# Performance work log

Measured on AMD Instinct MI355X. Metric: run time of the kernel, lower is better.

The kernel has to match this reference:

```python
import jax, jax.numpy as jnp
import numpy as np

N = 50000
IN_CH = 128
OUT_CH = 64
H1, C1 = 8, 8


def gat_layer(x, src, dst, W, att_src, att_dst, bias, heads, out_ch, concat, n_nodes):
    # x: [N, F_in]; W: [F_in, heads*out_ch]; att_*: [heads, out_ch]; bias: [heads*out_ch] or [out_ch]
    h = (x @ W).reshape(n_nodes, heads, out_ch)              # [N,H,C]
    a_src = jnp.einsum('nhc,hc->nh', h, att_src)             # [N,H]
    a_dst = jnp.einsum('nhc,hc->nh', h, att_dst)             # [N,H]
    e = jax.nn.leaky_relu(a_src[src] + a_dst[dst], 0.2)      # [E,H]
    # segment softmax over incoming edges of each dst node
    m = jax.ops.segment_max(e, dst, num_segments=n_nodes)    # [N,H]
    p = jnp.exp(e - m[dst])                                  # [E,H]
    s = jax.ops.segment_sum(p, dst, num_segments=n_nodes)    # [N,H]
    alpha = p / (s[dst] + 1e-16)                             # [E,H]
    out = jax.ops.segment_sum(h[src] * alpha[:, :, None], dst, num_segments=n_nodes)  # [N,H,C]
    out = out.reshape(n_nodes, heads * out_ch) if concat else out.mean(axis=1)
    return out + bias


def setup_inputs() -> dict:
    key = jax.random.key(0)
    ks = jax.random.split(key, 12)
    E = 1600000
    x = jax.random.normal(ks[0], (N, IN_CH), dtype=jnp.float32)
    edge_index = jax.random.randint(ks[1], (2, E), 0, N, dtype=jnp.int64)
    sc = 0.1
    return {
        'x': x,
        'edge_index': edge_index,
        'W1': jax.random.normal(ks[2], (IN_CH, H1 * C1), dtype=jnp.float32) * sc,
        'att_src1': jax.random.normal(ks[3], (H1, C1), dtype=jnp.float32) * sc,
        'att_dst1': jax.random.normal(ks[4], (H1, C1), dtype=jnp.float32) * sc,
        'b1': jnp.zeros((H1 * C1,), dtype=jnp.float32),
        'W2': jax.random.normal(ks[5], (H1 * C1, OUT_CH), dtype=jnp.float32) * sc,
        'att_src2': jax.random.normal(ks[6], (1, OUT_CH), dtype=jnp.float32) * sc,
        'att_dst2': jax.random.normal(ks[7], (1, OUT_CH), dtype=jnp.float32) * sc,
        'b2': jnp.zeros((OUT_CH,), dtype=jnp.float32),
        'lin_W': jax.random.normal(ks[8], (OUT_CH, 1), dtype=jnp.float32) * sc,
        'lin_b': jnp.zeros((1,), dtype=jnp.float32),
    }


def reference(x, edge_index, W1, att_src1, att_dst1, b1, W2, att_src2, att_dst2, b2, lin_W, lin_b):
    # add self loops (PyG GATConv default)
    loops = jnp.arange(N, dtype=edge_index.dtype)
    src = jnp.concatenate([edge_index[0], loops])
    dst = jnp.concatenate([edge_index[1], loops])
    # dropout layers are identity in eval mode
    h = gat_layer(x, src, dst, W1, att_src1, att_dst1, b1, H1, C1, True, N)
    h = jax.nn.elu(h)
    h = gat_layer(h, src, dst, W2, att_src2, att_dst2, b2, 1, OUT_CH, False, N)
    return h @ lin_W + lin_b
```

## Files before the change

### kernel.cpp

```cpp
#include <hip/hip_runtime.h>
#include <hip/hip_bf16.h>
#include <math.h>

#define NN     50000
#define FIN    128
#define F1     64
#define NH1    8
#define F2     64

#define BSH    256
#define NB     ((NN + BSH - 1) / BSH)
#define BCAP   9472
#define PREB   13
#define MG1B   ((NN + 255) / 256)

typedef __bf16 bf16x8 __attribute__((ext_vector_type(8)));
typedef float  f32x4  __attribute__((ext_vector_type(4)));


__device__ __forceinline__ float loadF(const void* p, long long i, int fp32) {
    if (fp32) return ((const float*)p)[i];
    return __bfloat162float(((const __hip_bfloat16*)p)[i]);
}
__device__ __forceinline__ int loadI_nt(const void* p, long long i, int i64) {
    if (i64) return (int)__builtin_nontemporal_load(&((const long long*)p)[i]);
    return __builtin_nontemporal_load(&((const int*)p)[i]);
}
__device__ __forceinline__ unsigned short f2bfu(float f) {
    unsigned u = __float_as_uint(f);
    return (unsigned short)((u + 0x7FFFu + ((u >> 16) & 1u)) >> 16);
}
__device__ __forceinline__ float b2f(unsigned short u) {
    return __uint_as_float(((unsigned)u) << 16);
}


__global__ __launch_bounds__(1024) void k_front(
    const void* __restrict__ x, const void* __restrict__ ei, int E, int Etot,
    int* __restrict__ flags,
    const void* __restrict__ W1, const void* __restrict__ W2,
    unsigned short* __restrict__ W1p, unsigned short* __restrict__ W2p,
    int* __restrict__ bcnt, unsigned* __restrict__ binned) {
    __shared__ int s_a, s_b;
    __shared__ int hist[NB], gbase[NB];
    int tid = threadIdx.x;
    if (blockIdx.x < PREB) {
        if (tid == 0) { s_a = 0; s_b = 0; }
        __syncthreads();
        const unsigned short* u = (const unsigned short*)x;
        int cnt = 0;
        for (int i = tid; i < 8192; i += 1024) {
            unsigned short v = u[i];
            if ((v & 0x7F80) == 0x7F80) cnt++;
        }
        if (cnt) atomicAdd(&s_a, cnt);
        const unsigned* e32 = (const unsigned*)ei;
        int nz = 0;
        for (int i = tid; i < 2048; i += 1024) {
            if (e32[2 * i + 1] != 0u) nz++;
        }
        if (nz) atomicAdd(&s_b, nz);
        __syncthreads();
        int fp32 = (s_a > 2) ? 1 : 0;
        if (tid == 0 && blockIdx.x == 0) {
            flags[0] = fp32;
            flags[1] = (s_b == 0) ? 1 : 0;
        }
        int gt = blockIdx.x * 1024 + tid, gs = PREB * 1024;
        for (int i = gt; i < (FIN / 32) * 4 * 512; i += gs) {
            int j = i & 7, l = (i >> 3) & 63, f = i >> 9;
            int kb = f >> 2, nt = f & 3;
            int k = kb * 32 + (l >> 4) * 8 + j, n = nt * 16 + (l & 15);
            W1p[i] = f2bfu(loadF(W1, k * 64 + n, fp32));
        }
        for (int i = gt; i < (F1 / 32) * 4 * 512; i += gs) {
            int j = i & 7, l = (i >> 3) & 63, f = i >> 9;
            int kb = f >> 2, nt = f & 3;
            int k = kb * 32 + (l >> 4) * 8 + j, n = nt * 16 + (l & 15);
            W2p[i] = f2bfu(loadF(W2, k * 64 + n, fp32));
        }
    } else {
        if (tid == 0) s_b = 0;
        for (int i = tid; i < NB; i += 1024) hist[i] = 0;
        __syncthreads();
        const unsigned* e32 = (const unsigned*)ei;
        int nz = 0;
        for (int i = tid; i < 2048; i += 1024) {
            if (e32[2 * i + 1] != 0u) nz++;
        }
        if (nz) atomicAdd(&s_b, nz);
        __syncthreads();
        int i64 = (s_b == 0) ? 1 : 0;
        long long base = (long long)(blockIdx.x - PREB) * 8192;
        unsigned pk[8]; short bb[8];
        #pragma unroll
        for (int u = 0; u < 8; ++u) {
            long long j = base + u * 1024 + tid;
            int s = -1, d = -1;
            if (j < Etot) {
                if (j < E) { s = loadI_nt(ei, j, i64); d = loadI_nt(ei, (long long)E + j, i64); }
                else       { s = d = (int)(j - E); }
            }
            if ((unsigned)s < NN && (unsigned)d < NN) {
                bb[u] = (short)(d >> 8);
                pk[u] = ((unsigned)s << 8) | (unsigned)(d & 255);
                atomicAdd(&hist[bb[u]], 1);
            } else bb[u] = -1;
        }
        __syncthreads();
        for (int i = tid; i < NB; i += 1024) {
            int h = hist[i];
            gbase[i] = h ? atomicAdd(&bcnt[i], h) : 0;
            hist[i] = 0;
        }
        __syncthreads();
        #pragma unroll
        for (int u = 0; u < 8; ++u) {
            if (bb[u] >= 0) {
                int pos = gbase[bb[u]] + atomicAdd(&hist[bb[u]], 1);
                if (pos < BCAP) binned[(size_t)bb[u] * BCAP + pos] = pk[u];
            }
        }
    }
}


__global__ __launch_bounds__(1024) void k_mid(
    const int* __restrict__ bcnt, const unsigned* __restrict__ binned,
    int* __restrict__ offs, int* __restrict__ perm,
    const void* __restrict__ x, const unsigned short* __restrict__ W1p,
    const void* __restrict__ attS, const void* __restrict__ attD,
    __hip_bfloat16* __restrict__ h1, float* __restrict__ a1s,
    float* __restrict__ a1d, const int* __restrict__ flags) {
    __shared__ __align__(16) char smem[33280];
    int tid = threadIdx.x;
    if (blockIdx.x < NB) {
        int* hist = (int*)smem;
        int* cur  = (int*)(smem + 1024);
        int* sd   = (int*)(smem + 2048);
        int bk = blockIdx.x;
        int n0 = bk * BSH;
        if (tid < 256) sd[tid] = (tid < NB) ? min(bcnt[tid], BCAP) : 0;
        __syncthreads();
        for (int off = 1; off < BSH; off <<= 1) {
            int t = 0;
            if (tid < 256 && tid >= off) t = sd[tid - off];
            __syncthreads();
            if (tid < 256) sd[tid] += t;
            __syncthreads();
        }
        int gb = (bk > 0) ? sd[bk - 1] : 0;
        if (bk == 0 && tid == 0) offs[NN] = sd[NB - 1];
        __syncthreads();
        int cnt = bcnt[bk]; if (cnt > BCAP) cnt = BCAP;
        const unsigned* bp = binned + (size_t)bk * BCAP;
        if (tid < 256) hist[tid] = 0;
        __syncthreads();
        for (int i = tid; i < cnt; i += 1024)
            atomicAdd(&hist[bp[i] & 255], 1);
        __syncthreads();
        int myh = (tid < 256) ? hist[tid] : 0;
        if (tid < 256) sd[tid] = myh;
        __syncthreads();
        for (int off = 1; off < BSH; off <<= 1) {
            int t = 0;
            if (tid < 256 && tid >= off) t = sd[tid - off];
            __syncthreads();
            if (tid < 256) sd[tid] += t;
            __syncthreads();
        }
        if (tid < 256) {
            int excl = sd[tid] - myh;
            cur[tid] = gb + excl;
            if (n0 + tid < NN) offs[n0 + tid] = gb + excl;
        }
        __syncthreads();
        for (int i = tid; i < cnt; i += 1024) {
            unsigned pk = bp[i];
            int pos = atomicAdd(&cur[pk & 255], 1);
            perm[pos] = (int)(pk >> 8);
        }
    } else {
        int fp32 = flags[0];
        unsigned short* hl = (unsigned short*)smem;
        float* attSl = (float*)(smem + 32768);
        float* attDl = (float*)(smem + 32768 + 256);
        if (tid < 64) { attSl[tid] = loadF(attS, tid, fp32); attDl[tid] = loadF(attD, tid, fp32); }
        int sub = tid >> 8, t = tid & 255;
        int w = t >> 6, l = t & 63;
        int quad = l >> 4, lm = l & 15;
        int n0 = (blockIdx.x - NB) * 256 + sub * 64;
        unsigned short* hls = hl + sub * 4096;

        bf16x8 bfr[16];
        #pragma unroll
        for (int f = 0; f < 16; ++f)
            bfr[f] = *(const bf16x8*)(W1p + f * 512 + l * 8);

        int nodeA = n0 + w * 16 + lm;
        long long rowA = (nodeA < NN) ? nodeA : 0;
        f32x4 acc[4];
        #pragma unroll
        for (int nt = 0; nt < 4; ++nt) acc[nt] = (f32x4){0.f, 0.f, 0.f, 0.f};

        #pragma unroll
        for (int kb = 0; kb < 4; ++kb) {
            bf16x8 af;
            if (!fp32) {
                af = *(const bf16x8*)((const unsigned short*)x + rowA * FIN + kb * 32 + quad * 8);
            } else {
                const float* xf = (const float*)x + rowA * FIN + kb * 32 + quad * 8;
                union { unsigned short s[8]; bf16x8 v; } tmp;
                #pragma unroll
                for (int j = 0; j < 8; ++j) tmp.s[j] = f2bfu(xf[j]);
                af = tmp.v;
            }
            #pragma unroll
            for (int nt = 0; nt < 4; ++nt)
                acc[nt] = __builtin_amdgcn_mfma_f32_16x16x32_bf16(af, bfr[kb * 4 + nt], acc[nt], 0, 0, 0);
        }

        #pragma unroll
        for (int nt = 0; nt < 4; ++nt) {
            #pragma unroll
            for (int r = 0; r < 4; ++r) {
                int nl = w * 16 + quad * 4 + r;
                int node = n0 + nl;
                int c = nt * 16 + lm;
                unsigned short hb = f2bfu(acc[nt][r]);
                hls[nl * 64 + c] = hb;
                if (node < NN) ((unsigned short*)h1)[(size_t)node * 64 + c] = hb;
            }
        }
        __syncthreads();
        #pragma unroll
        for (int pp = 0; pp < 2; ++pp) {
            int p = t + pp * 256;
            int nl = p >> 3, g = p & 7;
            int node = n0 + nl;
            float ss = 0.f, dd = 0.f;
            #pragma unroll
            for (int j = 0; j < 8; ++j) {
                float hv = b2f(hls[nl * 64 + g * 8 + j]);
                ss += hv * attSl[g * 8 + j];
                dd += hv * attDl[g * 8 + j];
            }
            if (node < NN) {
                a1s[(size_t)node * NH1 + g] = ss;
                a1d[(size_t)node * NH1 + g] = dd;
            }
        }
    }
}


#define HLP 72

__global__ __launch_bounds__(256) void k_agg1f(
    const int* __restrict__ offs, const int* __restrict__ perm,
    const __hip_bfloat16* __restrict__ h1, const float* __restrict__ a1s,
    const float* __restrict__ a1d, const void* __restrict__ b1,
    const unsigned short* __restrict__ W2p,
    const void* __restrict__ attS2, const void* __restrict__ attD2,
    const void* __restrict__ linW,
    float2* __restrict__ g2s, float* __restrict__ a2d,
    int n, const int* __restrict__ flags) {
    int fp32 = flags[0];
    __shared__ unsigned short hl[16 * HLP];
    __shared__ float attSl[64], attDl[64];
    __shared__ float sp[16 * 4], dp[16 * 4], gp[16 * 4];
    int tid = threadIdx.x;
    if (tid < 64) { attSl[tid] = loadF(attS2, tid, fp32); attDl[tid] = loadF(attD2, tid, fp32); }
    int w = tid >> 6, c = tid & 63;
    int n0 = blockIdx.x * 16;
    int u = c & 7, h = c >> 3, cb = c & 56;
    const unsigned short* hu = (const unsigned short*)h1;

    for (int m = 0; m < 4; ++m) {
        int d = n0 + w * 4 + m;
        if (d < n) {
            int start = offs[d], end = offs[d + 1];
            float adl = a1d[(size_t)d * NH1 + h];
            float acc = 0.f, denp = 0.f;
            for (int i = start; i < end; i += 8) {
                int j = i + u;
                int jc = (j < end) ? j : (end - 1);
                int sj = perm[jc];
                float e = a1s[(size_t)sj * NH1 + h] + adl;
                e = fmaxf(e, 0.2f * e);
                float p = (j < end) ? __expf(e) : 0.f;
                denp += p;
                #pragma unroll
                for (int k = 0; k < 8; ++k) {
                    int su = __builtin_amdgcn_readlane(sj, k);
                    float pk = __shfl(p, cb + k, 64);
                    acc = fmaf(pk, b2f(hu[(size_t)su * 64 + c]), acc);
                }
            }
            denp += __shfl_xor(denp, 1, 64);
            denp += __shfl_xor(denp, 2, 64);
            denp += __shfl_xor(denp, 4, 64);
            float v = acc / (denp + 1e-16f) + loadF(b1, c, fp32);
            v = (v > 0.f) ? v : expm1f(v);
            hl[(w * 4 + m) * HLP + c] = f2bfu(v);
        }
    }
    __syncthreads();

    int quad = c >> 4, lm = c & 15;
    bf16x8 bf0 = *(const bf16x8*)(W2p + (0 * 4 + w) * 512 + c * 8);
    bf16x8 bf1 = *(const bf16x8*)(W2p + (1 * 4 + w) * 512 + c * 8);
    bf16x8 af0 = *(const bf16x8*)(hl + lm * HLP + 0 * 32 + quad * 8);
    bf16x8 af1 = *(const bf16x8*)(hl + lm * HLP + 1 * 32 + quad * 8);
    f32x4 acc2 = (f32x4){0.f, 0.f, 0.f, 0.f};
    acc2 = __builtin_amdgcn_mfma_f32_16x16x32_bf16(af0, bf0, acc2, 0, 0, 0);
    acc2 = __builtin_amdgcn_mfma_f32_16x16x32_bf16(af1, bf1, acc2, 0, 0, 0);

    int cg = w * 16 + lm;
    float aSc = attSl[cg], aDc = attDl[cg];
    float lWc = loadF(linW, cg, fp32);
    #pragma unroll
    for (int r = 0; r < 4; ++r) {
        int nl = quad * 4 + r;
        unsigned short hb = f2bfu(acc2[r]);
        float hv = b2f(hb);
        float pvs = hv * aSc, pvd = hv * aDc, pvg = hv * lWc;
        pvs += __shfl_xor(pvs, 1, 64); pvd += __shfl_xor(pvd, 1, 64); pvg += __shfl_xor(pvg, 1, 64);
        pvs += __shfl_xor(pvs, 2, 64); pvd += __shfl_xor(pvd, 2, 64); pvg += __shfl_xor(pvg, 2, 64);
        pvs += __shfl_xor(pvs, 4, 64); pvd += __shfl_xor(pvd, 4, 64); pvg += __shfl_xor(pvg, 4, 64);
        pvs += __shfl_xor(pvs, 8, 64); pvd += __shfl_xor(pvd, 8, 64); pvg += __shfl_xor(pvg, 8, 64);
        if (lm == 0) { sp[nl * 4 + w] = pvs; dp[nl * 4 + w] = pvd; gp[nl * 4 + w] = pvg; }
    }
    __syncthreads();
    if (tid < 16) {
        int node = n0 + tid;
        if (node < n) {
            float ss = sp[tid * 4 + 0] + sp[tid * 4 + 1] + sp[tid * 4 + 2] + sp[tid * 4 + 3];
            float dd = dp[tid * 4 + 0] + dp[tid * 4 + 1] + dp[tid * 4 + 2] + dp[tid * 4 + 3];
            float gg = gp[tid * 4 + 0] + gp[tid * 4 + 1] + gp[tid * 4 + 2] + gp[tid * 4 + 3];
            g2s[node] = make_float2(ss, gg);
            a2d[node] = dd;
        }
    }
}


__global__ __launch_bounds__(256) void k_agg2(
    const int* __restrict__ offs, const int* __restrict__ perm,
    const float2* __restrict__ g2s, const float* __restrict__ a2d,
    const void* __restrict__ b2, const void* __restrict__ linW,
    const void* __restrict__ linb,
    void* __restrict__ out, int n, const int* __restrict__ flags) {
    int fp32 = flags[0];
    int w = threadIdx.x >> 6, c = threadIdx.x & 63;
    int d = blockIdx.x * 4 + w;
    if (d >= n) return;
    int start = offs[d], end = offs[d + 1];
    float ad = a2d[d];
    float acc = 0.f, den = 0.f;
    for (int i = start + c; i < end; i += 64) {
        int s = perm[i];
        float2 ag = g2s[s];
        float e = ag.x + ad;
        e = fmaxf(e, 0.2f * e);
        float p = __expf(e);
        acc = fmaf(p, ag.y, acc);
        den += p;
    }
    float cst = loadF(b2, c, fp32) * loadF(linW, c, fp32);
    #pragma unroll
    for (int off = 1; off < 64; off <<= 1) {
        acc += __shfl_xor(acc, off, 64);
        den += __shfl_xor(den, off, 64);
        cst += __shfl_xor(cst, off, 64);
    }
    if (c == 0) {
        float r = acc / (den + 1e-16f) + cst + loadF(linb, 0, fp32);
        if (fp32) ((float*)out)[d] = r;
        else      ((__hip_bfloat16*)out)[d] = __float2bfloat16(r);
    }
}


static inline char* carve(char*& p, size_t bytes) {
    char* r = p;
    p += (bytes + 255) & ~size_t(255);
    return r;
}

extern "C" void kernel_launch(void* const* d_in, const int* in_sizes, int n_in,
                              void* d_out, int out_size, void* d_ws, size_t ws_size,
                              hipStream_t stream) {
    const void* x     = d_in[0];
    const void* ei    = d_in[1];
    const void* W1    = d_in[2];
    const void* attS1 = d_in[3];
    const void* attD1 = d_in[4];
    const void* b1    = d_in[5];
    const void* W2    = d_in[6];
    const void* attS2 = d_in[7];
    const void* attD2 = d_in[8];
    const void* b2    = d_in[9];
    const void* linW  = d_in[10];
    const void* linb  = d_in[11];

    int E    = in_sizes[1] / 2;
    int Etot = E + NN;

    char* p = (char*)d_ws;
    int*   flags = (int*)carve(p, 256);
    int*   bcnt  = (int*)carve(p, (size_t)NB * 4);
    unsigned short* W1p = (unsigned short*)carve(p, 8192 * 2);
    unsigned short* W2p = (unsigned short*)carve(p, 4096 * 2);
    int*   offs  = (int*)carve(p, (size_t)(NN + 1) * 4);
    int*   perm  = (int*)carve(p, (size_t)Etot * 4);
    unsigned* binned = (unsigned*)carve(p, (size_t)NB * BCAP * 4);
    float*    a1s    = (float*)carve(p, (size_t)NN * NH1 * 4);
    float*    a1d    = (float*)carve(p, (size_t)NN * NH1 * 4);
    __hip_bfloat16* h1 = (__hip_bfloat16*)carve(p, (size_t)NN * F1 * 2);
    float2* g2s = (float2*)carve(p, (size_t)NN * 8);
    float*  a2d = (float*)carve(p, (size_t)NN * 4);

    hipMemsetAsync(bcnt, 0, (size_t)NB * 4, stream);

    int nbin = (Etot + 8191) / 8192;
    k_front<<<PREB + nbin, 1024, 0, stream>>>(x, ei, E, Etot, flags,
                                              W1, W2, W1p, W2p, bcnt, binned);
    k_mid<<<NB + MG1B, 1024, 0, stream>>>(bcnt, binned, offs, perm,
                                          x, W1p, attS1, attD1, h1, a1s, a1d, flags);
    k_agg1f<<<(NN + 15) / 16, 256, 0, stream>>>(offs, perm, h1, a1s, a1d, b1,
                                                W2p, attS2, attD2, linW, g2s, a2d, NN, flags);
    k_agg2<<<(NN + 3) / 4, 256, 0, stream>>>(offs, perm, g2s, a2d, b2, linW, linb, d_out, NN, flags);
}
```

Before: 202.5 us.

## Vectorize layer-1 aggregation: each lane loads 8 bf16 features per edge

```diff
diff --git a/kernel.cpp b/kernel.cpp
--- a/kernel.cpp
+++ b/kernel.cpp
@@ -16,6 +16,7 @@
 
 typedef __bf16 bf16x8 __attribute__((ext_vector_type(8)));
 typedef float  f32x4  __attribute__((ext_vector_type(4)));
+typedef unsigned short u16x8 __attribute__((ext_vector_type(8)));
 
 
 __device__ __forceinline__ float loadF(const void* p, long long i, int fp32) {
@@ -266,43 +267,65 @@
     float2* __restrict__ g2s, float* __restrict__ a2d,
     int n, const int* __restrict__ flags) {
     int fp32 = flags[0];
-    __shared__ unsigned short hl[16 * HLP];
+    __shared__ __align__(16) unsigned short hl[16 * HLP];
     __shared__ float attSl[64], attDl[64];
     __shared__ float sp[16 * 4], dp[16 * 4], gp[16 * 4];
     int tid = threadIdx.x;
     if (tid < 64) { attSl[tid] = loadF(attS2, tid, fp32); attDl[tid] = loadF(attD2, tid, fp32); }
     int w = tid >> 6, c = tid & 63;
     int n0 = blockIdx.x * 16;
-    int u = c & 7, h = c >> 3, cb = c & 56;
     const unsigned short* hu = (const unsigned short*)h1;
+
+    int g = c >> 3, q = c & 7;
+    float b1r[8];
+    #pragma unroll
+    for (int k = 0; k < 8; ++k) b1r[k] = loadF(b1, q * 8 + k, fp32);
 
     for (int m = 0; m < 4; ++m) {
         int d = n0 + w * 4 + m;
         if (d < n) {
             int start = offs[d], end = offs[d + 1];
-            float adl = a1d[(size_t)d * NH1 + h];
-            float acc = 0.f, denp = 0.f;
+            float adl = a1d[(size_t)d * NH1 + q];
+            float accv[8];
+            #pragma unroll
+            for (int k = 0; k < 8; ++k) accv[k] = 0.f;
+            float den = 0.f;
             for (int i = start; i < end; i += 8) {
-                int j = i + u;
+                int j = i + g;
                 int jc = (j < end) ? j : (end - 1);
                 int sj = perm[jc];
-                float e = a1s[(size_t)sj * NH1 + h] + adl;
+                float e = a1s[(size_t)sj * NH1 + q] + adl;
                 e = fmaxf(e, 0.2f * e);
                 float p = (j < end) ? __expf(e) : 0.f;
-                denp += p;
+                den += p;
+                u16x8 hv = *(const u16x8*)(hu + (size_t)sj * 64 + q * 8);
                 #pragma unroll
-                for (int k = 0; k < 8; ++k) {
-                    int su = __builtin_amdgcn_readlane(sj, k);
-                    float pk = __shfl(p, cb + k, 64);
-                    acc = fmaf(pk, b2f(hu[(size_t)su * 64 + c]), acc);
+                for (int k = 0; k < 8; ++k)
+                    accv[k] = fmaf(p, b2f(hv[k]), accv[k]);
+            }
+            #pragma unroll
+            for (int k = 0; k < 8; ++k) {
+                accv[k] += __shfl_xor(accv[k], 8, 64);
+                accv[k] += __shfl_xor(accv[k], 16, 64);
+                accv[k] += __shfl_xor(accv[k], 32, 64);
+            }
+            den += __shfl_xor(den, 8, 64);
+            den += __shfl_xor(den, 16, 64);
+            den += __shfl_xor(den, 32, 64);
+            float rden = 1.f / (den + 1e-16f);
+            if (g == 0) {
+                unsigned pk4[4];
+                #pragma unroll
+                for (int k = 0; k < 4; ++k) {
+                    float v0 = fmaf(accv[2 * k],     rden, b1r[2 * k]);
+                    float v1 = fmaf(accv[2 * k + 1], rden, b1r[2 * k + 1]);
+                    v0 = (v0 > 0.f) ? v0 : expm1f(v0);
+                    v1 = (v1 > 0.f) ? v1 : expm1f(v1);
+                    pk4[k] = (unsigned)f2bfu(v0) | ((unsigned)f2bfu(v1) << 16);
                 }
-            }
-            denp += __shfl_xor(denp, 1, 64);
-            denp += __shfl_xor(denp, 2, 64);
-            denp += __shfl_xor(denp, 4, 64);
-            float v = acc / (denp + 1e-16f) + loadF(b1, c, fp32);
-            v = (v > 0.f) ? v : expm1f(v);
-            hl[(w * 4 + m) * HLP + c] = f2bfu(v);
+                *(uint4*)&hl[(w * 4 + m) * HLP + q * 8] =
+                    make_uint4(pk4[0], pk4[1], pk4[2], pk4[3]);
+            }
         }
     }
     __syncthreads();
```

Measured after the change: 201.0 us. Within noise of the previous version (-0.8%).

## Restructure layer-1 aggregation to interleave four nodes with vectorized bf16 gathers

Applied to the files above, without the earlier changes.

```diff
diff --git a/kernel.cpp b/kernel.cpp
--- a/kernel.cpp
+++ b/kernel.cpp
@@ -16,6 +16,8 @@
 
 typedef __bf16 bf16x8 __attribute__((ext_vector_type(8)));
 typedef float  f32x4  __attribute__((ext_vector_type(4)));
+typedef float  f32x2  __attribute__((ext_vector_type(2)));
+typedef unsigned short u16x8 __attribute__((ext_vector_type(8)));
 
 
 __device__ __forceinline__ float loadF(const void* p, long long i, int fp32) {
@@ -256,7 +258,42 @@
 
 #define HLP 72
 
-__global__ __launch_bounds__(256) void k_agg1f(
+#define MACB(At, Uv, pv) { \
+    union { u16x8 v; unsigned u[4]; } U_; U_.v = Uv; \
+    f32x2 P_ = (f32x2){pv, pv}; \
+    _Pragma("unroll") \
+    for (int k = 0; k < 4; ++k) { \
+        f32x2 h_ = (f32x2){__uint_as_float(U_.u[k] << 16), \
+                           __uint_as_float(U_.u[k] & 0xFFFF0000u)}; \
+        At[k] = __builtin_elementwise_fma(P_, h_, At[k]); } }
+
+#define FIN(At, dnt, tt) { \
+    float av_[8]; \
+    _Pragma("unroll") \
+    for (int k = 0; k < 4; ++k) { av_[2*k] = At[k].x; av_[2*k+1] = At[k].y; } \
+    _Pragma("unroll") \
+    for (int k = 0; k < 8; ++k) { \
+        av_[k] += __shfl_xor(av_[k], 8, 64); \
+        av_[k] += __shfl_xor(av_[k], 16, 64); \
+        av_[k] += __shfl_xor(av_[k], 32, 64); } \
+    float dn_ = dnt; \
+    dn_ += __shfl_xor(dn_, 8, 64); \
+    dn_ += __shfl_xor(dn_, 16, 64); \
+    dn_ += __shfl_xor(dn_, 32, 64); \
+    float rd_ = 1.f / (dn_ + 1e-16f); \
+    if (g == 0) { \
+        unsigned pk4_[4]; \
+        _Pragma("unroll") \
+        for (int k = 0; k < 4; ++k) { \
+            float v0_ = fmaf(av_[2*k],   rd_, loadF(b1, q * 8 + 2*k,     fp32)); \
+            float v1_ = fmaf(av_[2*k+1], rd_, loadF(b1, q * 8 + 2*k + 1, fp32)); \
+            v0_ = (v0_ > 0.f) ? v0_ : expm1f(v0_); \
+            v1_ = (v1_ > 0.f) ? v1_ : expm1f(v1_); \
+            pk4_[k] = (unsigned)f2bfu(v0_) | ((unsigned)f2bfu(v1_) << 16); } \
+        *(uint4*)&hl[(w * 4 + tt) * HLP + q * 8] = \
+            make_uint4(pk4_[0], pk4_[1], pk4_[2], pk4_[3]); } }
+
+__global__ __launch_bounds__(256, 4) void k_agg1f(
     const int* __restrict__ offs, const int* __restrict__ perm,
     const __hip_bfloat16* __restrict__ h1, const float* __restrict__ a1s,
     const float* __restrict__ a1d, const void* __restrict__ b1,
@@ -266,45 +303,69 @@
     float2* __restrict__ g2s, float* __restrict__ a2d,
     int n, const int* __restrict__ flags) {
     int fp32 = flags[0];
-    __shared__ unsigned short hl[16 * HLP];
+    __shared__ __align__(16) unsigned short hl[16 * HLP];
     __shared__ float attSl[64], attDl[64];
     __shared__ float sp[16 * 4], dp[16 * 4], gp[16 * 4];
     int tid = threadIdx.x;
     if (tid < 64) { attSl[tid] = loadF(attS2, tid, fp32); attDl[tid] = loadF(attD2, tid, fp32); }
     int w = tid >> 6, c = tid & 63;
     int n0 = blockIdx.x * 16;
-    int u = c & 7, h = c >> 3, cb = c & 56;
     const unsigned short* hu = (const unsigned short*)h1;
 
-    for (int m = 0; m < 4; ++m) {
-        int d = n0 + w * 4 + m;
-        if (d < n) {
-            int start = offs[d], end = offs[d + 1];
-            float adl = a1d[(size_t)d * NH1 + h];
-            float acc = 0.f, denp = 0.f;
-            for (int i = start; i < end; i += 8) {
-                int j = i + u;
-                int jc = (j < end) ? j : (end - 1);
-                int sj = perm[jc];
-                float e = a1s[(size_t)sj * NH1 + h] + adl;
-                e = fmaxf(e, 0.2f * e);
-                float p = (j < end) ? __expf(e) : 0.f;
-                denp += p;
-                #pragma unroll
-                for (int k = 0; k < 8; ++k) {
-                    int su = __builtin_amdgcn_readlane(sj, k);
-                    float pk = __shfl(p, cb + k, 64);
-                    acc = fmaf(pk, b2f(hu[(size_t)su * 64 + c]), acc);
-                }
-            }
-            denp += __shfl_xor(denp, 1, 64);
-            denp += __shfl_xor(denp, 2, 64);
-            denp += __shfl_xor(denp, 4, 64);
-            float v = acc / (denp + 1e-16f) + loadF(b1, c, fp32);
-            v = (v > 0.f) ? v : expm1f(v);
-            hl[(w * 4 + m) * HLP + c] = f2bfu(v);
-        }
-    }
+    int g = c >> 3, q = c & 7;
+    int d0 = n0 + w * 4;
+    int o0 = offs[d0], o1 = offs[d0 + 1], o2 = offs[d0 + 2],
+        o3 = offs[d0 + 3], o4 = offs[d0 + 4];
+    int la0 = o1 - 1, la1 = o2 - 1, la2 = o3 - 1, la3 = o4 - 1;
+    int bt0 = o0 + g, bt1 = o1 + g, bt2 = o2 + g, bt3 = o3 + g;
+    float ad0 = a1d[(size_t)d0 * NH1 + q];
+    float ad1 = a1d[(size_t)(d0 + 1) * NH1 + q];
+    float ad2 = a1d[(size_t)(d0 + 2) * NH1 + q];
+    float ad3 = a1d[(size_t)(d0 + 3) * NH1 + q];
+    f32x2 A0[4], A1[4], A2[4], A3[4];
+    #pragma unroll
+    for (int k = 0; k < 4; ++k) {
+        A0[k] = (f32x2){0.f, 0.f}; A1[k] = (f32x2){0.f, 0.f};
+        A2[k] = (f32x2){0.f, 0.f}; A3[k] = (f32x2){0.f, 0.f};
+    }
+    float dn0 = 0.f, dn1 = 0.f, dn2 = 0.f, dn3 = 0.f;
+
+    int maxlen = max(max(o1 - o0, o2 - o1), max(o3 - o2, o4 - o3));
+    int niter = (maxlen + 7) >> 3;
+
+    for (int it = 0; it < niter; ++it) {
+        int j0 = bt0, j1 = bt1, j2 = bt2, j3 = bt3;
+        bt0 += 8; bt1 += 8; bt2 += 8; bt3 += 8;
+        int s0 = perm[min(j0, la0)];
+        int s1 = perm[min(j1, la1)];
+        int s2 = perm[min(j2, la2)];
+        int s3 = perm[min(j3, la3)];
+        float w0 = a1s[(size_t)s0 * NH1 + q];
+        float w1 = a1s[(size_t)s1 * NH1 + q];
+        float w2 = a1s[(size_t)s2 * NH1 + q];
+        float w3 = a1s[(size_t)s3 * NH1 + q];
+        u16x8 v0 = *(const u16x8*)(hu + (size_t)s0 * 64 + q * 8);
+        u16x8 v1 = *(const u16x8*)(hu + (size_t)s1 * 64 + q * 8);
+        u16x8 v2 = *(const u16x8*)(hu + (size_t)s2 * 64 + q * 8);
+        u16x8 v3 = *(const u16x8*)(hu + (size_t)s3 * 64 + q * 8);
+        float e0 = w0 + ad0; e0 = fmaxf(e0, 0.2f * e0);
+        float p0 = (j0 <= la0) ? __expf(e0) : 0.f; dn0 += p0;
+        float e1 = w1 + ad1; e1 = fmaxf(e1, 0.2f * e1);
+        float p1 = (j1 <= la1) ? __expf(e1) : 0.f; dn1 += p1;
+        float e2 = w2 + ad2; e2 = fmaxf(e2, 0.2f * e2);
+        float p2 = (j2 <= la2) ? __expf(e2) : 0.f; dn2 += p2;
+        float e3 = w3 + ad3; e3 = fmaxf(e3, 0.2f * e3);
+        float p3 = (j3 <= la3) ? __expf(e3) : 0.f; dn3 += p3;
+        MACB(A0, v0, p0)
+        MACB(A1, v1, p1)
+        MACB(A2, v2, p2)
+        MACB(A3, v3, p3)
+    }
+
+    FIN(A0, dn0, 0)
+    FIN(A1, dn1, 1)
+    FIN(A2, dn2, 2)
+    FIN(A3, dn3, 3)
     __syncthreads();
 
     int quad = c >> 4, lm = c & 15;
```

Measured after the change: 216.7 us. +7.0%, slower.
